# Optimization experiments

Hardware: AMD Instinct MI355X
Metric: run time of the kernel (lower is better)

Reference implementation:

```python
import jax, jax.numpy as jnp
import numpy as np

B, N, IN_DIM, OUT_DIM, HEADS = 4, 1024, 128, 128, 8
D = OUT_DIM // HEADS  # per-head dim = 16


def setup_inputs() -> dict:
    key = jax.random.key(0)
    k1, k2, k3, k4 = jax.random.split(key, 4)
    x = jax.random.normal(k1, (B, N, IN_DIM), dtype=jnp.float32)
    adj = jax.random.randint(k2, (B, N, N), 0, 2).astype(jnp.float32)
    W = jax.random.normal(k3, (IN_DIM, OUT_DIM), dtype=jnp.float32) * (IN_DIM ** -0.5)
    a = jax.random.normal(k4, (2 * D, 1), dtype=jnp.float32) * ((2 * D) ** -0.5)
    return {"x": x, "adj": adj, "W": W, "a": a}


def reference(x, adj, W, a):
    Bv, Nv, _ = x.shape
    # adj = clamp(adj + I, 0, 1); used only as a 0/1 mask
    mask = jnp.clip(adj + jnp.eye(Nv, dtype=adj.dtype)[None], 0.0, 1.0) > 0  # (B,N,N)
    xt = (x @ W).reshape(Bv, Nv, HEADS, D)  # (B,N,H,D)
    # a([x_i, x_j]) == x_i @ a_src + x_j @ a_dst  (exact decomposition of concat+linear)
    a_src, a_dst = a[:D, 0], a[D:, 0]
    src = jnp.einsum('bnhd,d->bnh', xt, a_src)
    dst = jnp.einsum('bnhd,d->bnh', xt, a_dst)
    e = jax.nn.leaky_relu(src[:, :, None, :] + dst[:, None, :, :], negative_slope=0.2)  # (B,i,j,H)
    m = mask[..., None]  # (B,N,N,1) broadcast over heads
    neg_inf = jnp.asarray(-jnp.inf, e.dtype)
    # max over neighbors j (dim=2), detached, diagonal guarantees >=1 valid entry
    mx = jax.lax.stop_gradient(jnp.max(jnp.where(m, e, neg_inf), axis=2, keepdims=True))
    # Faithful to torch code: masked entries become 0 (NOT -inf) before softmax,
    # so they contribute exp(0)=1 to the softmax, exactly as in the original.
    e_stable = jnp.where(m, e - mx, jnp.zeros((), e.dtype))
    alpha = jax.nn.softmax(e_stable, axis=2)  # (B,i,j,H)
    h = jnp.einsum('bijh,bjhd->bihd', alpha, xt).reshape(Bv, Nv, HEADS * D)  # concat=True
    return jax.nn.relu(h)
```

## Files before the change

kernel.cpp:

```cpp
#include <hip/hip_runtime.h>
#include <hip/hip_bf16.h>
#include <math.h>
#include <stdint.h>

#define BV 4
#define NV 1024
#define IND 128
#define OUTD 128
#define NH 8
#define DD 16

typedef __attribute__((ext_vector_type(8))) short bf16x8;
typedef __attribute__((ext_vector_type(4))) float f32x4;

__device__ __forceinline__ ushort bf16rne(float f) {
    uint32_t u = __float_as_uint(f);
    u += 0x7fff + ((u >> 16) & 1);
    return (ushort)(u >> 16);
}

__device__ __forceinline__ uint32_t cvtpk_bf16(float lo, float hi) {
    uint32_t r;
    asm("v_cvt_pk_bf16_f32 %0, %1, %2" : "=v"(r) : "v"(lo), "v"(hi));
    return r;
}

__global__ __launch_bounds__(256) void kA(
    const float* __restrict__ x, const float* __restrict__ adj,
    const float* __restrict__ W, const float* __restrict__ a,
    uint32_t* __restrict__ bits, ushort* __restrict__ xhi,
    float* __restrict__ src, float* __restrict__ dst_t)
{
    const int pid = blockIdx.x;
    const int tid = threadIdx.x;

    if (pid >= 512) {
        const int row = pid - 512;
        const int i = row & (NV - 1);
        const int wave = tid >> 6, lane = tid & 63;
        const float* arow = adj + (size_t)row * NV;
        #pragma unroll
        for (int r = 0; r < 4; ++r) {
            const int j = (r * 4 + wave) * 64 + lane;
            const bool m = (arow[j] > 0.f) || (j == i);
            const unsigned long long bal = __ballot(m);
            if (lane == 0) {
                bits[(size_t)row * 32 + (r * 4 + wave) * 2]     = (uint32_t)bal;
                bits[(size_t)row * 32 + (r * 4 + wave) * 2 + 1] = (uint32_t)(bal >> 32);
            }
        }
        return;
    }

    const int jt = pid & 15, bh = pid >> 4;
    const int b = bh >> 3, h = bh & 7;
    const int j0 = jt * 64;
    const int jl = tid >> 2, dq = tid & 3;
    const int gj = b * NV + j0 + jl;

    float acc0 = 0.f, acc1 = 0.f, acc2 = 0.f, acc3 = 0.f;
    const float* xrow = x + (size_t)gj * IND;
    const float* wcol = W + h * DD + dq * 4;

    #pragma unroll
    for (int kc = 0; kc < IND; kc += 32) {
        float4 xr[8];
        #pragma unroll
        for (int u = 0; u < 8; ++u)
            xr[u] = *(const float4*)&xrow[kc + u * 4];
        #pragma unroll
        for (int u = 0; u < 8; ++u) {
            #pragma unroll
            for (int v = 0; v < 4; ++v) {
                const float xs = ((const float*)&xr[u])[v];
                const float4 w = *(const float4*)&wcol[(size_t)(kc + u * 4 + v) * OUTD];
                acc0 = fmaf(xs, w.x, acc0);
                acc1 = fmaf(xs, w.y, acc1);
                acc2 = fmaf(xs, w.z, acc2);
                acc3 = fmaf(xs, w.w, acc3);
            }
        }
    }

    {
        const int d0 = dq * 4;
        float s = acc0 * a[d0] + acc1 * a[d0 + 1] + acc2 * a[d0 + 2] + acc3 * a[d0 + 3];
        float t = acc0 * a[DD + d0] + acc1 * a[DD + d0 + 1] + acc2 * a[DD + d0 + 2] + acc3 * a[DD + d0 + 3];
        s += __shfl_xor(s, 1); s += __shfl_xor(s, 2);
        t += __shfl_xor(t, 1); t += __shfl_xor(t, 2);
        if (dq == 0) {
            src[(size_t)gj * NH + h] = s;
            dst_t[(size_t)bh * NV + j0 + jl] = t;
        }
    }

    __shared__ ushort thi[16][80];
    {
        const float av[4] = {acc0, acc1, acc2, acc3};
        #pragma unroll
        for (int i2 = 0; i2 < 4; ++i2)
            thi[dq * 4 + i2][jl] = bf16rne(av[i2]);
    }
    __syncthreads();
    if (tid < 128) {
        const int d = tid >> 3, jo = tid & 7;
        const uint4 vh = *(const uint4*)&thi[d][jo * 8];
        const size_t base = ((size_t)(bh * 16 + d)) * NV + j0 + jo * 8;
        *(uint4*)&xhi[base] = vh;
    }
}

__global__ __launch_bounds__(256, 6) void kB(
    const uint32_t* __restrict__ bits, const ushort* __restrict__ xhi,
    const float* __restrict__ dst_t, const float* __restrict__ src,
    float* __restrict__ out)
{
    const int bid = blockIdx.x;
    const int xcd = bid & 7, t2 = (bid >> 3) & 3, it = bid >> 5;
    const int bh = xcd * 4 + t2;
    const int b = bh >> 3, h = bh & 7;
    const int i0 = it * 16;

    const int tid = threadIdx.x;
    const int jq = tid >> 6, lane = tid & 63;
    const int g = lane >> 4, r16 = lane & 15;

    __shared__ float dstl[NV];
    __shared__ float mxr[4][16];
    __shared__ float red_acc[3][64][4];
    __shared__ float red_den[3][64];

    {
        const float4* gd = (const float4*)(dst_t + (size_t)bh * NV);
        *(float4*)&dstl[tid * 4] = gd[tid];
    }
    const int grow = b * NV + i0 + r16;
    const float srcv = src[(size_t)grow * NH + h];
    uint32_t blw[8];
    #pragma unroll
    for (int s = 0; s < 8; ++s)
        blw[s] = bits[(size_t)grow * 32 + jq * 8 + s];
    __syncthreads();

    float dmax = -INFINITY;
    #pragma unroll
    for (int s = 0; s < 8; ++s) {
        const int base = jq * 256 + s * 32 + g * 8;
        const uint32_t bb = (blw[s] >> (g * 8)) & 0xffu;
        const float4 v0 = *(const float4*)&dstl[base];
        const float4 v1 = *(const float4*)&dstl[base + 4];
        const float dv[8] = {v0.x, v0.y, v0.z, v0.w, v1.x, v1.y, v1.z, v1.w};
        #pragma unroll
        for (int t = 0; t < 8; ++t) {
            const float sel = (bb & (1u << t)) ? dv[t] : -INFINITY;
            dmax = fmaxf(dmax, sel);
        }
    }
    dmax = fmaxf(dmax, __shfl_xor(dmax, 16));
    dmax = fmaxf(dmax, __shfl_xor(dmax, 32));
    if (g == 0) mxr[jq][r16] = dmax;
    __syncthreads();
    dmax = fmaxf(fmaxf(mxr[0][r16], mxr[1][r16]), fmaxf(mxr[2][r16], mxr[3][r16]));
    const float S = srcv + dmax;
    const float mxv = fmaxf(S, 0.2f * S);

    f32x4 acc = {0.f, 0.f, 0.f, 0.f};
    float den0 = 0.f, den1 = 0.f;
    const ushort* xrow = xhi + ((size_t)(bh * 16 + r16)) * NV;
    #pragma unroll
    for (int s = 0; s < 8; ++s) {
        const int base = jq * 256 + s * 32 + g * 8;
        const uint32_t bb = (blw[s] >> (g * 8)) & 0xffu;
        const float4 v0 = *(const float4*)&dstl[base];
        const float4 v1 = *(const float4*)&dstl[base + 4];
        const float dv[8] = {v0.x, v0.y, v0.z, v0.w, v1.x, v1.y, v1.z, v1.w};
        union { uint32_t u[4]; bf16x8 v; } af;
        #pragma unroll
        for (int p = 0; p < 4; ++p) {
            float e0 = srcv + dv[2 * p];
            float e1 = srcv + dv[2 * p + 1];
            e0 = fmaxf(e0, 0.2f * e0);
            e1 = fmaxf(e1, 0.2f * e1);
            const float x0 = __expf(e0 - mxv);
            const float x1 = __expf(e1 - mxv);
            const float w0 = (bb & (1u << (2 * p))) ? x0 : 1.0f;
            const float w1 = (bb & (1u << (2 * p + 1))) ? x1 : 1.0f;
            den0 += w0;
            den1 += w1;
            af.u[p] = cvtpk_bf16(w0, w1);
        }
        const bf16x8 vh = *(const bf16x8*)&xrow[base];
        acc = __builtin_amdgcn_mfma_f32_16x16x32_bf16(af.v, vh, acc, 0, 0, 0);
    }
    float den = den0 + den1;

    if (jq > 0) {
        *(float4*)&red_acc[jq - 1][lane][0] = *(float4*)&acc;
        red_den[jq - 1][lane] = den;
    }
    __syncthreads();
    if (jq == 0) {
        #pragma unroll
        for (int qq = 0; qq < 3; ++qq) {
            const float4 oa = *(const float4*)&red_acc[qq][lane][0];
            acc[0] += oa.x; acc[1] += oa.y; acc[2] += oa.z; acc[3] += oa.w;
            den += red_den[qq][lane];
        }
        den += __shfl_xor(den, 16);
        den += __shfl_xor(den, 32);
        #pragma unroll
        for (int q = 0; q < 4; ++q) {
            const int orow = g * 4 + q;
            const float dq = __shfl(den, orow);
            float rv = acc[q] / dq;
            rv = fmaxf(rv, 0.f);
            out[((size_t)(b * NV) + i0 + orow) * OUTD + h * 16 + r16] = rv;
        }
    }
}

extern "C" void kernel_launch(void* const* d_in, const int* in_sizes, int n_in,
                              void* d_out, int out_size, void* d_ws, size_t ws_size,
                              hipStream_t stream)
{
    const float* x   = (const float*)d_in[0];
    const float* adj = (const float*)d_in[1];
    const float* W   = (const float*)d_in[2];
    const float* a   = (const float*)d_in[3];
    float* out = (float*)d_out;

    char* ws = (char*)d_ws;
    ushort* xhi    = (ushort*)ws;
    float* dst_t   = (float*)(ws + 1024 * 1024);
    float* src     = (float*)(ws + 1024 * 1024 + 128 * 1024);
    uint32_t* bits = (uint32_t*)(ws + 1024 * 1024 + 256 * 1024);

    kA<<<512 + BV * NV, 256, 0, stream>>>(x, adj, W, a, bits, xhi, src, dst_t);
    kB<<<2048, 256, 0, stream>>>(bits, xhi, dst_t, src, out);
}
```

Measured before the change: 30.89 us.

## Prefetch value tiles early, use exp2 with prescaled logits, MFMA denominator

Stores src/dst logits pre-multiplied by log2(e) so the softmax can use the native exp2 instruction. All eight bf16 value fragments are loaded before the max pass so their latency overlaps it. The softmax denominator is now computed by a second MFMA against a ones matrix instead of scalar adds and shuffles, which also rounds the weights in the denominator to bf16 the same way as in the numerator. Occupancy hint drops from 6 to 4 blocks per CU to make room for the extra registers the prefetch needs.

```diff
diff --git a/kernel.cpp b/kernel.cpp
--- a/kernel.cpp
+++ b/kernel.cpp
@@ -9,6 +9,7 @@
 #define OUTD 128
 #define NH 8
 #define DD 16
+#define LOG2E 1.4426950408889634f
 
 typedef __attribute__((ext_vector_type(8))) short bf16x8;
 typedef __attribute__((ext_vector_type(4))) float f32x4;
@@ -24,6 +25,12 @@
     asm("v_cvt_pk_bf16_f32 %0, %1, %2" : "=v"(r) : "v"(lo), "v"(hi));
     return r;
 }
+
+#if __has_builtin(__builtin_amdgcn_exp2f)
+#define EXP2(x) __builtin_amdgcn_exp2f(x)
+#else
+#define EXP2(x) __expf((x) * 0.6931471805599453f)
+#endif
 
 __global__ __launch_bounds__(256) void kA(
     const float* __restrict__ x, const float* __restrict__ adj,
@@ -89,8 +96,8 @@
         s += __shfl_xor(s, 1); s += __shfl_xor(s, 2);
         t += __shfl_xor(t, 1); t += __shfl_xor(t, 2);
         if (dq == 0) {
-            src[(size_t)gj * NH + h] = s;
-            dst_t[(size_t)bh * NV + j0 + jl] = t;
+            src[(size_t)gj * NH + h] = s * LOG2E;
+            dst_t[(size_t)bh * NV + j0 + jl] = t * LOG2E;
         }
     }
 
@@ -110,7 +117,7 @@
     }
 }
 
-__global__ __launch_bounds__(256, 6) void kB(
+__global__ __launch_bounds__(256, 4) void kB(
     const uint32_t* __restrict__ bits, const ushort* __restrict__ xhi,
     const float* __restrict__ dst_t, const float* __restrict__ src,
     float* __restrict__ out)
@@ -128,7 +135,7 @@
     __shared__ float dstl[NV];
     __shared__ float mxr[4][16];
     __shared__ float red_acc[3][64][4];
-    __shared__ float red_den[3][64];
+    __shared__ float red_den[3][64][4];
 
     {
         const float4* gd = (const float4*)(dst_t + (size_t)bh * NV);
@@ -140,6 +147,16 @@
     #pragma unroll
     for (int s = 0; s < 8; ++s)
         blw[s] = bits[(size_t)grow * 32 + jq * 8 + s];
+
+    const ushort* xrow = xhi + ((size_t)(bh * 16 + r16)) * NV;
+    bf16x8 vh0 = *(const bf16x8*)&xrow[jq * 256 + 0 * 32 + g * 8];
+    bf16x8 vh1 = *(const bf16x8*)&xrow[jq * 256 + 1 * 32 + g * 8];
+    bf16x8 vh2 = *(const bf16x8*)&xrow[jq * 256 + 2 * 32 + g * 8];
+    bf16x8 vh3 = *(const bf16x8*)&xrow[jq * 256 + 3 * 32 + g * 8];
+    bf16x8 vh4 = *(const bf16x8*)&xrow[jq * 256 + 4 * 32 + g * 8];
+    bf16x8 vh5 = *(const bf16x8*)&xrow[jq * 256 + 5 * 32 + g * 8];
+    bf16x8 vh6 = *(const bf16x8*)&xrow[jq * 256 + 6 * 32 + g * 8];
+    bf16x8 vh7 = *(const bf16x8*)&xrow[jq * 256 + 7 * 32 + g * 8];
     __syncthreads();
 
     float dmax = -INFINITY;
@@ -164,9 +181,10 @@
     const float S = srcv + dmax;
     const float mxv = fmaxf(S, 0.2f * S);
 
-    f32x4 acc = {0.f, 0.f, 0.f, 0.f};
-    float den0 = 0.f, den1 = 0.f;
-    const ushort* xrow = xhi + ((size_t)(bh * 16 + r16)) * NV;
+    union { uint32_t u[4]; bf16x8 v; } ones;
+    ones.u[0] = ones.u[1] = ones.u[2] = ones.u[3] = 0x3f803f80u;
+    f32x4 acc  = {0.f, 0.f, 0.f, 0.f};
+    f32x4 accd = {0.f, 0.f, 0.f, 0.f};
     #pragma unroll
     for (int s = 0; s < 8; ++s) {
         const int base = jq * 256 + s * 32 + g * 8;
@@ -181,38 +199,36 @@
             float e1 = srcv + dv[2 * p + 1];
             e0 = fmaxf(e0, 0.2f * e0);
             e1 = fmaxf(e1, 0.2f * e1);
-            const float x0 = __expf(e0 - mxv);
-            const float x1 = __expf(e1 - mxv);
+            const float x0 = EXP2(e0 - mxv);
+            const float x1 = EXP2(e1 - mxv);
             const float w0 = (bb & (1u << (2 * p))) ? x0 : 1.0f;
             const float w1 = (bb & (1u << (2 * p + 1))) ? x1 : 1.0f;
-            den0 += w0;
-            den1 += w1;
             af.u[p] = cvtpk_bf16(w0, w1);
         }
-        const bf16x8 vh = *(const bf16x8*)&xrow[base];
-        acc = __builtin_amdgcn_mfma_f32_16x16x32_bf16(af.v, vh, acc, 0, 0, 0);
-    }
-    float den = den0 + den1;
+        const bf16x8 vb = (s == 0) ? vh0 : (s == 1) ? vh1 : (s == 2) ? vh2 :
+                          (s == 3) ? vh3 : (s == 4) ? vh4 : (s == 5) ? vh5 :
+                          (s == 6) ? vh6 : vh7;
+        acc  = __builtin_amdgcn_mfma_f32_16x16x32_bf16(af.v, vb, acc, 0, 0, 0);
+        accd = __builtin_amdgcn_mfma_f32_16x16x32_bf16(af.v, ones.v, accd, 0, 0, 0);
+    }
 
     if (jq > 0) {
         *(float4*)&red_acc[jq - 1][lane][0] = *(float4*)&acc;
-        red_den[jq - 1][lane] = den;
+        *(float4*)&red_den[jq - 1][lane][0] = *(float4*)&accd;
     }
     __syncthreads();
     if (jq == 0) {
         #pragma unroll
         for (int qq = 0; qq < 3; ++qq) {
             const float4 oa = *(const float4*)&red_acc[qq][lane][0];
-            acc[0] += oa.x; acc[1] += oa.y; acc[2] += oa.z; acc[3] += oa.w;
-            den += red_den[qq][lane];
-        }
-        den += __shfl_xor(den, 16);
-        den += __shfl_xor(den, 32);
+            const float4 od = *(const float4*)&red_den[qq][lane][0];
+            acc[0] += oa.x;  acc[1] += oa.y;  acc[2] += oa.z;  acc[3] += oa.w;
+            accd[0] += od.x; accd[1] += od.y; accd[2] += od.z; accd[3] += od.w;
+        }
         #pragma unroll
         for (int q = 0; q < 4; ++q) {
             const int orow = g * 4 + q;
-            const float dq = __shfl(den, orow);
-            float rv = acc[q] / dq;
+            float rv = acc[q] / accd[q];
             rv = fmaxf(rv, 0.f);
             out[((size_t)(b * NV) + i0 + orow) * OUTD + h * 16 + r16] = rv;
         }
```

Result: slower. 32.61 us (+5.6%).
